# Kernel optimization log

Hardware: AMD Instinct MI355X
Metric: run time of the kernel (lower is better)

The kernel has to match this reference:

```python
import jax, jax.numpy as jnp
import numpy as np

NUM_EMBEDDINGS = 1024
EMBEDDING_DIM = 256


def setup_inputs() -> dict:
    key = jax.random.key(0)
    kx, kw = jax.random.split(key)
    x = jax.random.normal(kx, (64, 32, 32, EMBEDDING_DIM), dtype=jnp.float32)
    # nn.Embedding default init: N(0, 1)
    embedding_weight = jax.random.normal(kw, (NUM_EMBEDDINGS, EMBEDDING_DIM), dtype=jnp.float32)
    return {"x": x, "embedding_weight": embedding_weight}


def reference(x, embedding_weight):
    D = embedding_weight.shape[1]
    x_flat = x.reshape(-1, D)  # [N, D]
    distances = (
        jnp.sum(x_flat * x_flat, axis=1, keepdims=True)
        + jnp.sum(embedding_weight * embedding_weight, axis=1)
        - 2.0 * jnp.matmul(x_flat, embedding_weight.T)
    )
    indices = jnp.argmin(distances, axis=1)  # [N]
    quantized = embedding_weight[indices].reshape(x.shape)
    return quantized, indices
```

## Files before the change

### kernel.cpp

```cpp
#include <hip/hip_runtime.h>


#define K_EMB  1024
#define D_DIM  256
#define N_ROWS 65536

typedef unsigned int u32;
typedef unsigned long long u64;
typedef __attribute__((ext_vector_type(8)))  _Float16 f16x8;
typedef __attribute__((ext_vector_type(4)))  _Float16 f16x4;
typedef __attribute__((ext_vector_type(16))) float    f32x16;

__device__ __forceinline__ u32 f32_sortable(float f) {
    u32 u = __float_as_uint(f);
    return u ^ ((u32)((int)u >> 31) | 0x80000000u);
}
__device__ __forceinline__ float f32_unsort(u32 u) {
    u32 v = (u & 0x80000000u) ? (u ^ 0x80000000u) : ~u;
    return __uint_as_float(v);
}

#define GLDS(gp, lp) __builtin_amdgcn_global_load_lds( \
    (const __attribute__((address_space(1))) void*)(gp), \
    (__attribute__((address_space(3))) void*)(lp), 16, 0, 0)

__global__ void vq_prep(const float* __restrict__ emb,
                        _Float16* __restrict__ ehi,
                        _Float16* __restrict__ cn2,
                        float* __restrict__ cnormf) {
    int gid = blockIdx.x * 256 + threadIdx.x;
    int code = gid >> 6, lane = gid & 63;
    float4 v = ((const float4*)(emb + (size_t)code * D_DIM))[lane];
    f16x4 hv = {(_Float16)v.x, (_Float16)v.y, (_Float16)v.z, (_Float16)v.w};
    ((f16x4*)(ehi + (size_t)code * D_DIM))[lane] = hv;
    float s = v.x * v.x + v.y * v.y + v.z * v.z + v.w * v.w;
    #pragma unroll
    for (int off = 32; off > 0; off >>= 1) s += __shfl_down(s, off, 64);
    if (lane == 0) {
        float cn = 0.5f * s;
        cnormf[code] = cn;
        _Float16 ch = (_Float16)cn;
        _Float16 cl = (_Float16)(cn - (float)ch);
        f16x8 e = {};
        e[0] = (_Float16)(-(float)ch);
        e[1] = (_Float16)(-(float)cl);
        ((f16x8*)cn2)[code] = e;
    }
}

__global__ __launch_bounds__(256, 2) void vq_main(
    const float* __restrict__ x, const float* __restrict__ emb,
    const _Float16* __restrict__ eh, const _Float16* __restrict__ cn2,
    const float* __restrict__ cnormf,
    float* __restrict__ outq, float* __restrict__ outi)
{
    __shared__ _Float16 T[2][2][8192];
    __shared__ u32 xchg[2][128][3];
    __shared__ int winners[128];

    const int t = threadIdx.x, w = t >> 6, lane = t & 63;
    const int m = lane & 31, kh = lane >> 5;
    const int p = w >> 1;
    const int h = w & 1;
    const int blkrow = blockIdx.x * 128;
    const int rowA = blkrow + p * 64 + m;
    const int kh4 = kh * 4;

    f16x8 bhA[16], bhB[16];
    {
        const float* xr = x + (size_t)rowA * D_DIM + kh * 8;
        #pragma unroll
        for (int s = 0; s < 16; s++) {
            float4 v0 = *(const float4*)(xr + s * 16);
            float4 v1 = *(const float4*)(xr + s * 16 + 4);
            bhA[s] = (f16x8){(_Float16)v0.x, (_Float16)v0.y, (_Float16)v0.z, (_Float16)v0.w,
                             (_Float16)v1.x, (_Float16)v1.y, (_Float16)v1.z, (_Float16)v1.w};
            float4 u0 = *(const float4*)(xr + 32 * D_DIM + s * 16);
            float4 u1 = *(const float4*)(xr + 32 * D_DIM + s * 16 + 4);
            bhB[s] = (f16x8){(_Float16)u0.x, (_Float16)u0.y, (_Float16)u0.z, (_Float16)u0.w,
                             (_Float16)u1.x, (_Float16)u1.y, (_Float16)u1.z, (_Float16)u1.w};
        }
    }
    f16x8 xe = {};
    if (kh == 0) { xe[0] = (_Float16)1.0f; xe[1] = (_Float16)1.0f; }

    u32 A1 = 0, A2 = 0, A3 = 0, B1 = 0, B2 = 0, B3 = 0;

    auto t3 = [](u32& c1, u32& c2, u32& c3, u32 pv) {
        u32 u2 = c1 < pv ? c1 : pv;
        u32 u3 = c2 < pv ? c2 : pv;
        c1 = c1 > pv ? c1 : pv;
        c2 = u2 > c2 ? u2 : c2;
        c3 = u3 > c3 ? u3 : c3;
    };

    auto stage = [&](int c) {
        const int buf = c & 1;
        #pragma unroll
        for (int hh = 0; hh < 2; hh++) {
            const _Float16* srcb = eh + (size_t)(hh * 512 + c * 32 + m) * D_DIM + (lane >> 5) * 8;
            _Float16* dstb = &T[buf][hh][0];
            #pragma unroll
            for (int i = 0; i < 4; i++) {
                int r = w * 4 + i;
                GLDS(srcb + r * 16, dstb + r * 512);
            }
        }
    };

    auto compute = [&](int buf, f32x16& a0, f32x16& a1, int c) {
        const f16x8* Af = (const f16x8*)&T[buf][h][0];
        f16x8 e = ((const f16x8*)cn2)[h * 512 + c * 32 + m];
        a0 = (f32x16){}; a1 = (f32x16){};
        #pragma unroll
        for (int s = 0; s < 16; s++) {
            f16x8 fa = Af[(2 * s + kh) * 32 + m];
            a0 = __builtin_amdgcn_mfma_f32_32x32x16_f16(fa, bhA[s], a0, 0, 0, 0);
            a1 = __builtin_amdgcn_mfma_f32_32x32x16_f16(fa, bhB[s], a1, 0, 0, 0);
        }
        a0 = __builtin_amdgcn_mfma_f32_32x32x16_f16(e, xe, a0, 0, 0, 0);
        a1 = __builtin_amdgcn_mfma_f32_32x32x16_f16(e, xe, a1, 0, 0, 0);
    };

    auto top3p = [&](const f32x16& a0, const f32x16& a1, int c) {
        const u32 sbase = (u32)(h * 512 + c * 32) + kh4;
        #pragma unroll
        for (int r = 0; r < 16; r++) {
            u32 code = sbase + (r & 3) + 8 * (r >> 2);
            u32 pa = (f32_sortable(a0[r]) & 0xFFFFFC00u) | code;
            t3(A1, A2, A3, pa);
            u32 pb = (f32_sortable(a1[r]) & 0xFFFFFC00u) | code;
            t3(B1, B2, B3, pb);
        }
    };

    f32x16 aA0, aA1, aB0, aB1;
    stage(0);
    for (int cc = 0; cc < 16; cc += 2) {
        __syncthreads();
        if (cc + 1 < 16) stage(cc + 1);
        compute(0, aA0, aA1, cc);
        if (cc) top3p(aB0, aB1, cc - 1);
        __syncthreads();
        if (cc + 2 < 16) stage(cc + 2);
        compute(1, aB0, aB1, cc + 1);
        top3p(aA0, aA1, cc);
    }
    top3p(aB0, aB1, 15);

    {
        u32 q1 = (u32)__shfl_xor((int)A1, 32, 64);
        u32 q2 = (u32)__shfl_xor((int)A2, 32, 64);
        u32 q3 = (u32)__shfl_xor((int)A3, 32, 64);
        t3(A1, A2, A3, q1); t3(A1, A2, A3, q2); t3(A1, A2, A3, q3);
        q1 = (u32)__shfl_xor((int)B1, 32, 64);
        q2 = (u32)__shfl_xor((int)B2, 32, 64);
        q3 = (u32)__shfl_xor((int)B3, 32, 64);
        t3(B1, B2, B3, q1); t3(B1, B2, B3, q2); t3(B1, B2, B3, q3);
    }

    if (kh == 0) {
        int ra = p * 64 + m;
        xchg[h][ra][0] = A1; xchg[h][ra][1] = A2; xchg[h][ra][2] = A3;
        xchg[h][ra + 32][0] = B1; xchg[h][ra + 32][1] = B2; xchg[h][ra + 32][2] = B3;
    }
    __syncthreads();

    const int rl = p * 64 + h * 32 + m;
    u32 c1 = 0, c2 = 0, c3 = 0;
    t3(c1, c2, c3, xchg[0][rl][0]); t3(c1, c2, c3, xchg[0][rl][1]); t3(c1, c2, c3, xchg[0][rl][2]);
    t3(c1, c2, c3, xchg[1][rl][0]); t3(c1, c2, c3, xchg[1][rl][1]); t3(c1, c2, c3, xchg[1][rl][2]);

    float s1f = f32_unsort(c1), s2f = f32_unsort(c2), s3f = f32_unsort(c3);
    u32 i1 = c1 & 1023u, i2 = c2 & 1023u, i3 = c3 & 1023u;
    bool need = (s1f - s2f) <= 0.25f;
    if (kh == 0 && !need) winners[rl] = (int)i1;
    u64 mask = __ballot(kh == 0 && need);
    while (mask) {
        int r = __ffsll((unsigned long long)mask) - 1;
        mask &= mask - 1;
        int row = blkrow + p * 64 + h * 32 + r;
        u32 d1 = (u32)__shfl((int)i1, r, 64);
        u32 d2 = (u32)__shfl((int)i2, r, 64);
        u32 d3 = (u32)__shfl((int)i3, r, 64);
        float g3 = __shfl(s1f - s3f, r, 64);
        int ncand = (g3 <= 0.25f) ? 3 : 2;
        float4 xv = ((const float4*)(x + (size_t)row * D_DIM))[lane];
        float bs = -3.0e38f; int bi = 0x7fffffff;
        u32 cand[3] = {d1, d2, d3};
        for (int q = 0; q < ncand; q++) {
            int ccd = (int)cand[q];
            float4 ev = ((const float4*)(emb + (size_t)ccd * D_DIM))[lane];
            float d = xv.x * ev.x + xv.y * ev.y + xv.z * ev.z + xv.w * ev.w;
            #pragma unroll
            for (int dd = 1; dd < 64; dd <<= 1) d += __shfl_xor(d, dd, 64);
            float sc = d - cnormf[ccd];
            if (sc > bs || (sc == bs && ccd < bi)) { bs = sc; bi = ccd; }
        }
        if (lane == 0) winners[p * 64 + h * 32 + r] = bi;
    }

    if (kh == 0) outi[blkrow + rl] = (float)winners[rl];
    const int gbase = p * 64 + h * 32;
    #pragma unroll 8
    for (int r = 0; r < 32; r++) {
        int idx = winners[gbase + r];
        int row = blkrow + gbase + r;
        float4 qv = ((const float4*)(emb + (size_t)idx * D_DIM))[lane];
        ((float4*)(outq + (size_t)row * D_DIM))[lane] = qv;
    }
}

extern "C" void kernel_launch(void* const* d_in, const int* in_sizes, int n_in,
                              void* d_out, int out_size, void* d_ws, size_t ws_size,
                              hipStream_t stream) {
    const float* x   = (const float*)d_in[0];
    const float* emb = (const float*)d_in[1];
    float* outq = (float*)d_out;
    float* outi = outq + (size_t)N_ROWS * D_DIM;

    _Float16* ehi = (_Float16*)d_ws;
    _Float16* cn2 = ehi + (size_t)K_EMB * D_DIM;
    float* cnormf = (float*)(cn2 + (size_t)K_EMB * 8);

    vq_prep<<<K_EMB / 4, 256, 0, stream>>>(emb, ehi, cn2, cnormf);
    vq_main<<<N_ROWS / 128, 256, 0, stream>>>(x, emb, ehi, cn2, cnormf,
                                              outq, outi);
}
```

Baseline: 165.8 us.

## Split work across 8 waves with one row tile per wave

Raises the main kernel's block from 256 to 512 threads so each wave owns one 32-row tile of x instead of two. This roughly halves per-wave registers (one accumulator and one x-fragment set) and raises occupancy, so more MFMA and load latency can be hidden. The manual two-stage software pipeline that overlapped compute with top-3 selection is replaced by a simple loop, and the codebook staging is split across all eight waves. The refinement and output-copy phases are re-mapped to 16 rows per wave. The trade-off is less instruction-level overlap inside each wave and more waves contending at each barrier.

```diff
diff --git a/kernel.cpp b/kernel.cpp
--- a/kernel.cpp
+++ b/kernel.cpp
@@ -48,7 +48,7 @@
     }
 }
 
-__global__ __launch_bounds__(256, 2) void vq_main(
+__global__ __launch_bounds__(512, 4) void vq_main(
     const float* __restrict__ x, const float* __restrict__ emb,
     const _Float16* __restrict__ eh, const _Float16* __restrict__ cn2,
     const float* __restrict__ cnormf,
@@ -63,28 +63,36 @@
     const int p = w >> 1;
     const int h = w & 1;
     const int blkrow = blockIdx.x * 128;
-    const int rowA = blkrow + p * 64 + m;
+    const int myrow = blkrow + p * 32 + m;
     const int kh4 = kh * 4;
 
-    f16x8 bhA[16], bhB[16];
+    auto stage = [&](int c) {
+        _Float16* dstb = &T[c & 1][h][0];
+        const _Float16* srcb = eh + (size_t)(h * 512 + c * 32 + m) * D_DIM + kh * 8;
+        #pragma unroll
+        for (int i = 0; i < 4; i++) {
+            int r = p * 4 + i;
+            GLDS(srcb + r * 16, dstb + r * 512);
+        }
+    };
+
+    stage(0);
+
+    f16x8 bh[16];
     {
-        const float* xr = x + (size_t)rowA * D_DIM + kh * 8;
+        const float* xr = x + (size_t)myrow * D_DIM + kh * 8;
         #pragma unroll
         for (int s = 0; s < 16; s++) {
             float4 v0 = *(const float4*)(xr + s * 16);
             float4 v1 = *(const float4*)(xr + s * 16 + 4);
-            bhA[s] = (f16x8){(_Float16)v0.x, (_Float16)v0.y, (_Float16)v0.z, (_Float16)v0.w,
-                             (_Float16)v1.x, (_Float16)v1.y, (_Float16)v1.z, (_Float16)v1.w};
-            float4 u0 = *(const float4*)(xr + 32 * D_DIM + s * 16);
-            float4 u1 = *(const float4*)(xr + 32 * D_DIM + s * 16 + 4);
-            bhB[s] = (f16x8){(_Float16)u0.x, (_Float16)u0.y, (_Float16)u0.z, (_Float16)u0.w,
-                             (_Float16)u1.x, (_Float16)u1.y, (_Float16)u1.z, (_Float16)u1.w};
+            bh[s] = (f16x8){(_Float16)v0.x, (_Float16)v0.y, (_Float16)v0.z, (_Float16)v0.w,
+                            (_Float16)v1.x, (_Float16)v1.y, (_Float16)v1.z, (_Float16)v1.w};
         }
     }
     f16x8 xe = {};
     if (kh == 0) { xe[0] = (_Float16)1.0f; xe[1] = (_Float16)1.0f; }
 
-    u32 A1 = 0, A2 = 0, A3 = 0, B1 = 0, B2 = 0, B3 = 0;
+    u32 A1 = 0, A2 = 0, A3 = 0;
 
     auto t3 = [](u32& c1, u32& c2, u32& c3, u32 pv) {
         u32 u2 = c1 < pv ? c1 : pv;
@@ -94,92 +102,59 @@
         c3 = u3 > c3 ? u3 : c3;
     };
 
-    auto stage = [&](int c) {
-        const int buf = c & 1;
-        #pragma unroll
-        for (int hh = 0; hh < 2; hh++) {
-            const _Float16* srcb = eh + (size_t)(hh * 512 + c * 32 + m) * D_DIM + (lane >> 5) * 8;
-            _Float16* dstb = &T[buf][hh][0];
-            #pragma unroll
-            for (int i = 0; i < 4; i++) {
-                int r = w * 4 + i;
-                GLDS(srcb + r * 16, dstb + r * 512);
-            }
-        }
-    };
-
-    auto compute = [&](int buf, f32x16& a0, f32x16& a1, int c) {
-        const f16x8* Af = (const f16x8*)&T[buf][h][0];
+    for (int c = 0; c < 16; ++c) {
+        __syncthreads();
+        if (c + 1 < 16) stage(c + 1);
+        const f16x8* Af = (const f16x8*)&T[c & 1][h][0];
         f16x8 e = ((const f16x8*)cn2)[h * 512 + c * 32 + m];
-        a0 = (f32x16){}; a1 = (f32x16){};
+        f32x16 a = {};
         #pragma unroll
         for (int s = 0; s < 16; s++) {
             f16x8 fa = Af[(2 * s + kh) * 32 + m];
-            a0 = __builtin_amdgcn_mfma_f32_32x32x16_f16(fa, bhA[s], a0, 0, 0, 0);
-            a1 = __builtin_amdgcn_mfma_f32_32x32x16_f16(fa, bhB[s], a1, 0, 0, 0);
-        }
-        a0 = __builtin_amdgcn_mfma_f32_32x32x16_f16(e, xe, a0, 0, 0, 0);
-        a1 = __builtin_amdgcn_mfma_f32_32x32x16_f16(e, xe, a1, 0, 0, 0);
-    };
-
-    auto top3p = [&](const f32x16& a0, const f32x16& a1, int c) {
+            a = __builtin_amdgcn_mfma_f32_32x32x16_f16(fa, bh[s], a, 0, 0, 0);
+        }
+        a = __builtin_amdgcn_mfma_f32_32x32x16_f16(e, xe, a, 0, 0, 0);
         const u32 sbase = (u32)(h * 512 + c * 32) + kh4;
         #pragma unroll
         for (int r = 0; r < 16; r++) {
             u32 code = sbase + (r & 3) + 8 * (r >> 2);
-            u32 pa = (f32_sortable(a0[r]) & 0xFFFFFC00u) | code;
-            t3(A1, A2, A3, pa);
-            u32 pb = (f32_sortable(a1[r]) & 0xFFFFFC00u) | code;
-            t3(B1, B2, B3, pb);
-        }
-    };
-
-    f32x16 aA0, aA1, aB0, aB1;
-    stage(0);
-    for (int cc = 0; cc < 16; cc += 2) {
-        __syncthreads();
-        if (cc + 1 < 16) stage(cc + 1);
-        compute(0, aA0, aA1, cc);
-        if (cc) top3p(aB0, aB1, cc - 1);
-        __syncthreads();
-        if (cc + 2 < 16) stage(cc + 2);
-        compute(1, aB0, aB1, cc + 1);
-        top3p(aA0, aA1, cc);
-    }
-    top3p(aB0, aB1, 15);
+            u32 pk = (f32_sortable(a[r]) & 0xFFFFFC00u) | code;
+            t3(A1, A2, A3, pk);
+        }
+    }
 
     {
         u32 q1 = (u32)__shfl_xor((int)A1, 32, 64);
         u32 q2 = (u32)__shfl_xor((int)A2, 32, 64);
         u32 q3 = (u32)__shfl_xor((int)A3, 32, 64);
         t3(A1, A2, A3, q1); t3(A1, A2, A3, q2); t3(A1, A2, A3, q3);
-        q1 = (u32)__shfl_xor((int)B1, 32, 64);
-        q2 = (u32)__shfl_xor((int)B2, 32, 64);
-        q3 = (u32)__shfl_xor((int)B3, 32, 64);
-        t3(B1, B2, B3, q1); t3(B1, B2, B3, q2); t3(B1, B2, B3, q3);
     }
 
     if (kh == 0) {
-        int ra = p * 64 + m;
+        int ra = p * 32 + m;
         xchg[h][ra][0] = A1; xchg[h][ra][1] = A2; xchg[h][ra][2] = A3;
-        xchg[h][ra + 32][0] = B1; xchg[h][ra + 32][1] = B2; xchg[h][ra + 32][2] = B3;
     }
     __syncthreads();
 
-    const int rl = p * 64 + h * 32 + m;
+    const int lr = w * 16 + (lane & 15);
     u32 c1 = 0, c2 = 0, c3 = 0;
-    t3(c1, c2, c3, xchg[0][rl][0]); t3(c1, c2, c3, xchg[0][rl][1]); t3(c1, c2, c3, xchg[0][rl][2]);
-    t3(c1, c2, c3, xchg[1][rl][0]); t3(c1, c2, c3, xchg[1][rl][1]); t3(c1, c2, c3, xchg[1][rl][2]);
+    #pragma unroll
+    for (int hh = 0; hh < 2; hh++) {
+        t3(c1, c2, c3, xchg[hh][lr][0]);
+        t3(c1, c2, c3, xchg[hh][lr][1]);
+        t3(c1, c2, c3, xchg[hh][lr][2]);
+    }
 
     float s1f = f32_unsort(c1), s2f = f32_unsort(c2), s3f = f32_unsort(c3);
     u32 i1 = c1 & 1023u, i2 = c2 & 1023u, i3 = c3 & 1023u;
+    const bool act = lane < 16;
     bool need = (s1f - s2f) <= 0.25f;
-    if (kh == 0 && !need) winners[rl] = (int)i1;
-    u64 mask = __ballot(kh == 0 && need);
+    if (act && !need) winners[lr] = (int)i1;
+    u64 mask = __ballot(act && need);
     while (mask) {
         int r = __ffsll((unsigned long long)mask) - 1;
         mask &= mask - 1;
-        int row = blkrow + p * 64 + h * 32 + r;
+        int row = blkrow + w * 16 + r;
         u32 d1 = (u32)__shfl((int)i1, r, 64);
         u32 d2 = (u32)__shfl((int)i2, r, 64);
         u32 d3 = (u32)__shfl((int)i3, r, 64);
@@ -197,15 +172,14 @@
             float sc = d - cnormf[ccd];
             if (sc > bs || (sc == bs && ccd < bi)) { bs = sc; bi = ccd; }
         }
-        if (lane == 0) winners[p * 64 + h * 32 + r] = bi;
-    }
-
-    if (kh == 0) outi[blkrow + rl] = (float)winners[rl];
-    const int gbase = p * 64 + h * 32;
+        if (lane == 0) winners[w * 16 + r] = bi;
+    }
+
+    if (act) outi[blkrow + lr] = (float)winners[lr];
     #pragma unroll 8
-    for (int r = 0; r < 32; r++) {
-        int idx = winners[gbase + r];
-        int row = blkrow + gbase + r;
+    for (int r = 0; r < 16; r++) {
+        int idx = winners[w * 16 + r];
+        int row = blkrow + w * 16 + r;
         float4 qv = ((const float4*)(emb + (size_t)idx * D_DIM))[lane];
         ((float4*)(outq + (size_t)row * D_DIM))[lane] = qv;
     }
@@ -224,6 +198,6 @@
     float* cnormf = (float*)(cn2 + (size_t)K_EMB * 8);
 
     vq_prep<<<K_EMB / 4, 256, 0, stream>>>(emb, ehi, cn2, cnormf);
-    vq_main<<<N_ROWS / 128, 256, 0, stream>>>(x, emb, ehi, cn2, cnormf,
+    vq_main<<<N_ROWS / 128, 512, 0, stream>>>(x, emb, ehi, cn2, cnormf,
                                               outq, outi);
 }
```

Result: no change. 164.4 us (-0.8%).
